# Performance work log

Hardware: AMD Instinct MI355X
Metric: run time of the kernel (lower is better)

## Reference

```python
import jax, jax.numpy as jnp
import numpy as np

B, N = 2, 4096
IN_CH, OUT_CH = 64, 64
L_MAX, NR = 3, 4
KERNEL_RADIUS = 0.5
PATCH = 64  # hardcoded in torch topk(-dist, 64)


def setup_inputs() -> dict:
    key = jax.random.key(0)
    k1, k2, k3 = jax.random.split(key, 3)
    xyz = jax.random.normal(k1, (B, N, 3), dtype=jnp.float32)
    signal = jax.random.normal(k2, (B, N, IN_CH), dtype=jnp.float32)
    # xavier_uniform on (out, in, nr, l_max+1): receptive = nr*(l_max+1)
    recept = NR * (L_MAX + 1)
    bound = float(np.sqrt(6.0 / (IN_CH * recept + OUT_CH * recept)))
    weight = jax.random.uniform(k3, (OUT_CH, IN_CH, NR, L_MAX + 1), dtype=jnp.float32,
                                minval=-bound, maxval=bound)
    biases = jnp.zeros((OUT_CH,), dtype=jnp.float32)
    return {"xyz": xyz, "signal": signal, "weight": weight, "biases": biases}


def _sph(X):
    # X: [B,N,P,3] l2-normalized patch directions -> [B,N,P,(L_MAX+1)^2]
    x, y, z = X[..., 0], X[..., 1], X[..., 2]
    x2, y2, z2 = x * x, y * y, z * z
    Ys = []
    Ys.append(jnp.full_like(x, 0.5 * np.sqrt(1.0 / np.pi)))           # Y00
    s3 = np.sqrt(3.0 / np.pi) / 2.0
    Ys += [s3 * y, s3 * z, -s3 * x]                                    # l=1
    s15h = np.sqrt(15.0 / np.pi) / 2.0
    s15q = np.sqrt(15.0 / np.pi) / 4.0
    s5q = np.sqrt(5.0 / np.pi) / 4.0
    Ys += [s15h * x * y, s15h * y * z, s5q * (2.0 * z2 - x2 - y2),
           -s15h * z * x, s15q * (x2 - y2)]                            # l=2
    c33 = np.sqrt(35.0 / (2.0 * np.pi)) / 4.0
    c32 = np.sqrt(105.0 / np.pi) / 2.0
    c31 = np.sqrt(21.0 / (2.0 * np.pi)) / 4.0
    c30 = np.sqrt(7.0 / np.pi) / 4.0
    c32b = np.sqrt(105.0 / np.pi) / 4.0
    Ys += [c33 * (3.0 * x2 * y - y * y2),
           c32 * x * y * z,
           c31 * (4.0 * y * z2 - x2 * y - y * y2),
           c30 * (2.0 * z * z2 - 3.0 * x2 * z - 3.0 * y2 * z),
           -c31 * (4.0 * z2 * x - x * x2 - x * y2),
           c32b * (x2 * z - y2 * z),
           -c33 * (x * x2 - 3.0 * x * y2)]                             # l=3
    return jnp.stack(Ys, axis=-1)


def reference(xyz, signal, weight, biases):
    # pairwise squared distances via matmul (costly_cdist)
    r2 = jnp.sum(xyz * xyz, axis=2)                                    # [B,N]
    sqd = r2[:, :, None] - 2.0 * jnp.einsum('bnd,bmd->bnm', xyz, xyz) + r2[:, None, :]
    neg_vals, idx = jax.lax.top_k(-sqd, PATCH)                         # KNN
    sq_patches_dist = -neg_vals                                        # [B,N,P]
    gather = jax.vmap(lambda pts, i: pts[i])                           # per-batch fancy gather
    patches = gather(xyz, idx) - xyz[:, :, None, :]                    # [B,N,P,3]
    # F.normalize(p=2, dim=-1, eps=0.01): x / max(||x||, eps)
    nrm = jnp.linalg.norm(patches, axis=-1, keepdims=True)
    Y = _sph(patches / jnp.maximum(nrm, 0.01))                         # [B,N,P,K2]
    dist = jnp.sqrt(jnp.maximum(sq_patches_dist, 1e-4))                # [B,N,P]
    r_grid = jnp.linspace(0.0, KERNEL_RADIUS, NR, dtype=jnp.float32)   # [NR]
    sigma = KERNEL_RADIUS / (NR - 1)
    rad = jnp.exp(-jnp.square(dist[..., None] - r_grid) / (2.0 * sigma ** 2))  # [B,N,P,NR]
    yk = Y[:, :, :, None, :] * rad[..., None]                          # [B,N,P,NR,K2]
    y_w = jnp.sum(yk[:, :, :, 0, 0], axis=2)[:, :, None, None, None]   # [B,N,1,1,1]
    conv_kernel = yk / (y_w + 1e-6)
    sig_patches = gather(signal, idx)                                  # [B,N,P,C]
    y = jnp.einsum('bvprn,bvpc->bvcrn', conv_kernel, sig_patches)
    y = y * y
    bands = [jnp.sum(y[..., l * l:(l + 1) * (l + 1)], axis=-1) for l in range(L_MAX + 1)]
    y = jnp.stack(bands, axis=-1)                                      # [B,N,C,NR,L+1]
    y = jnp.sqrt(jnp.maximum(y, 1e-4))
    out = jnp.einsum('ijrn,bvjrn->bvi', weight, y) + biases
    return out
```

## Files before the change

### kernel.cpp

```cpp
#include <hip/hip_runtime.h>
#include <hip/hip_bf16.h>
#include <math.h>

#define NB 2
#define NPTS 4096
#define CH 64
#define PATCH 64

typedef __attribute__((ext_vector_type(8))) short s16x8;
typedef __attribute__((ext_vector_type(4))) short s16x4;
typedef __attribute__((ext_vector_type(4))) float f32x4;
typedef __attribute__((ext_vector_type(4))) unsigned u32x4;

static __device__ __forceinline__ short f2bf(float f) {
    union { __hip_bfloat16 h; short s; } u;
    u.h = __float2bfloat16(f);
    return u.s;
}

__global__ __launch_bounds__(256) void prep_kernel(const float* __restrict__ W,
                                                   short* __restrict__ Wfrag,
                                                   const float* __restrict__ xyz,
                                                   float4* __restrict__ xyz4) {
    const int bid = blockIdx.x;
    const int tid = threadIdx.x;
    if (bid < 32) {
        const int gid = bid * 256 + tid;
        const int mt = gid >> 11;
        const int st = (gid >> 6) & 31;
        const int l  = gid & 63;
        const int i  = mt * 16 + (l & 15);
        const int k0 = st * 32 + (l >> 4) * 8;
        const f32x4 a = *(const f32x4*)&W[i * 1024 + k0];
        const f32x4 c = *(const f32x4*)&W[i * 1024 + k0 + 4];
        s16x8 v;
        v[0] = f2bf(a[0]); v[1] = f2bf(a[1]); v[2] = f2bf(a[2]); v[3] = f2bf(a[3]);
        v[4] = f2bf(c[0]); v[5] = f2bf(c[1]); v[6] = f2bf(c[2]); v[7] = f2bf(c[3]);
        *(s16x8*)&Wfrag[gid * 8] = v;
    } else {
        const int idx = (bid - 32) * 256 + tid;
        float4 v;
        v.x = xyz[idx * 3 + 0];
        v.y = xyz[idx * 3 + 1];
        v.z = xyz[idx * 3 + 2];
        v.w = 0.0f;
        xyz4[idx] = v;
    }
}

__global__ __launch_bounds__(256, 6) void knn_kernel(const float4* __restrict__ xyz4,
                                                     int* __restrict__ knn_idx) {
    const int pt   = blockIdx.x;
    const int b    = pt >> 12;
    const int q    = pt & (NPTS - 1);
    const int tid  = threadIdx.x;
    const int wv   = tid >> 6;
    const int lane = tid & 63;

    __shared__ __align__(16) unsigned hist[4096];
    __shared__ __align__(16) unsigned short sbin[4096];
    __shared__ unsigned wsum[4];
    __shared__ unsigned sh_H;
    __shared__ int sh_need;
    __shared__ int cnt_less, cnt_tie;

    const float4* xb = xyz4 + (size_t)b * NPTS;
    const float4 qp = xb[q];

#pragma unroll
    for (int u = 0; u < 4; ++u)
        ((u32x4*)hist)[u * 256 + tid] = (u32x4){0u, 0u, 0u, 0u};
    if (tid == 0) { cnt_less = 0; cnt_tie = 0; }
    __syncthreads();

#pragma unroll 4
    for (int i = 0; i < 16; ++i) {
        const int m = i * 256 + tid;
        const float4 p = xb[m];
        const float dx = p.x - qp.x;
        const float dy = p.y - qp.y;
        const float dz = p.z - qp.z;
        const float sq = fmaf(dx, dx, fmaf(dy, dy, dz * dz));
        const unsigned hk = __float_as_uint(sq) >> 19;
        sbin[i * 256 + tid] = (unsigned short)hk;
        atomicAdd(&hist[hk], 1u);
    }
    __syncthreads();

    unsigned tsum = 0;
#pragma unroll
    for (int u = 0; u < 4; ++u) {
        const u32x4 h4 = ((const u32x4*)hist)[tid * 4 + u];
        tsum += h4[0] + h4[1] + h4[2] + h4[3];
    }
    unsigned run = tsum;
#pragma unroll
    for (int off = 1; off < 64; off <<= 1) {
        const unsigned v = __shfl_up(run, off);
        if (lane >= off) run += v;
    }
    if (lane == 63) wsum[wv] = run;
    __syncthreads();
    unsigned wbase = 0;
    for (int w2 = 0; w2 < wv; ++w2) wbase += wsum[w2];
    const unsigned incl = wbase + run;
    const unsigned excl = incl - tsum;
    if ((int)excl < PATCH && PATCH <= (int)incl) {
        int nrem = PATCH - (int)excl;
        for (int u = 0; u < 16; ++u) {
            const unsigned cb = hist[tid * 16 + u];
            if (nrem <= (int)cb) { sh_H = (unsigned)(tid * 16 + u); sh_need = nrem; break; }
            nrem -= (int)cb;
        }
    }
    __syncthreads();

    const unsigned H = sh_H;
    const int need  = sh_need;
    const int nless = PATCH - need;
    int* optr = knn_idx + (size_t)pt * PATCH;
    unsigned* ckey = hist;
    unsigned* cidx = hist + 2048;

#pragma unroll 4
    for (int i = 0; i < 16; ++i) {
        const int m = i * 256 + tid;
        const unsigned hk = sbin[i * 256 + tid];
        if (hk < H) {
            const int pos = atomicAdd(&cnt_less, 1);
            optr[pos] = m;
        } else if (hk == H) {
            const int pos = atomicAdd(&cnt_tie, 1);
            if (pos < 2048) {
                const float4 p = xb[m];
                const float dx = p.x - qp.x;
                const float dy = p.y - qp.y;
                const float dz = p.z - qp.z;
                const float sq = fmaf(dx, dx, fmaf(dy, dy, dz * dz));
                ckey[pos] = __float_as_uint(sq);
                cidx[pos] = m;
            }
        }
    }
    __syncthreads();

    const int nc = min(cnt_tie, 2048);
    for (int i = tid; i < nc; i += 256) {
        const unsigned ki = ckey[i];
        int rank = 0;
        for (int j = 0; j < nc; ++j) {
            const unsigned kj = ckey[j];
            rank += (kj < ki || (kj == ki && j < i)) ? 1 : 0;
        }
        if (rank < need) optr[nless + rank] = cidx[i];
    }
}

__global__ __launch_bounds__(256, 4) void conv_kernel(const float4* __restrict__ xyz4,
                                                      const float* __restrict__ signal,
                                                      const short* __restrict__ Wfrag,
                                                      const float* __restrict__ biases,
                                                      const int* __restrict__ knn_idx,
                                                      float* __restrict__ out) {
    const int tid  = threadIdx.x;
    const int wv   = tid >> 6;
    const int lane = tid & 63;
    const int ln15 = lane & 15;
    const int kq   = lane >> 4;

    __shared__ __align__(16) short cks_bf[4096];
    __shared__ __align__(16) short ckF[4096];
    __shared__ __align__(16) short sigF[4096];
    __shared__ __align__(16) short zb[4 * 1032];
    __shared__ int   sIdx[PATCH];
    __shared__ float sh_inv;

    for (int it = 0; it < 4; ++it) {
        const int pt = blockIdx.x * 4 + it;
        const int b  = pt >> 12;
        const int q  = pt & (NPTS - 1);

        if (tid < PATCH) sIdx[tid] = knn_idx[(size_t)pt * PATCH + tid];
        __syncthreads();

        if (wv == 0) {
            const int p   = lane;
            const int idx = sIdx[p];
            const float4 cp = xyz4[(size_t)b * NPTS + q];
            const float4 np = xyz4[(size_t)b * NPTS + idx];
            const float dx = np.x - cp.x;
            const float dy = np.y - cp.y;
            const float dz = np.z - cp.z;
            const float nrm2 = dx * dx + dy * dy + dz * dz;
            const float inv_n = 1.0f / fmaxf(sqrtf(nrm2), 0.01f);
            const float x = dx * inv_n, y = dy * inv_n, z = dz * inv_n;
            const float x2 = x * x, y2 = y * y, zz = z * z;

            float Y[16];
            Y[0] = 0.28209479177387814f;
            const float s3 = 0.4886025119029199f;
            Y[1] = s3 * y;  Y[2] = s3 * z;  Y[3] = -s3 * x;
            const float s15h = 1.0925484305920792f;
            const float s15q = 0.5462742152960396f;
            const float s5q  = 0.31539156525252005f;
            Y[4] = s15h * x * y;
            Y[5] = s15h * y * z;
            Y[6] = s5q * (2.0f * zz - x2 - y2);
            Y[7] = -s15h * z * x;
            Y[8] = s15q * (x2 - y2);
            const float c33  = 0.5900435899266435f;
            const float c32  = 2.8906114426405543f;
            const float c31  = 0.4570457994644658f;
            const float c30  = 0.3731763325901154f;
            const float c32b = 1.4453057213202771f;
            Y[9]  = c33 * (3.0f * x2 * y - y * y2);
            Y[10] = c32 * x * y * z;
            Y[11] = c31 * (4.0f * y * zz - x2 * y - y * y2);
            Y[12] = c30 * (2.0f * z * zz - 3.0f * x2 * z - 3.0f * y2 * z);
            Y[13] = -c31 * (4.0f * zz * x - x * x2 - x * y2);
            Y[14] = c32b * (x2 * z - y2 * z);
            Y[15] = -c33 * (x * x2 - 3.0f * x * y2);

            const float dist = sqrtf(fmaxf(nrm2, 1e-4f));
            const float d1 = dist - 0.16666667f;
            const float d2 = dist - 0.33333334f;
            const float d3 = dist - 0.5f;
            float rad[4];
            rad[0] = expf(-dist * dist * 18.0f);
            rad[1] = expf(-d1 * d1 * 18.0f);
            rad[2] = expf(-d2 * d2 * 18.0f);
            rad[3] = expf(-d3 * d3 * 18.0f);

            const int pm = p & 15;
#pragma unroll
            for (int chunk = 0; chunk < 16; ++chunk) {
                const int r  = chunk >> 2;
                const int kb = (chunk & 3) * 4;
                s16x4 v;
                v[0] = f2bf(Y[kb + 0] * rad[r]);
                v[1] = f2bf(Y[kb + 1] * rad[r]);
                v[2] = f2bf(Y[kb + 2] * rad[r]);
                v[3] = f2bf(Y[kb + 3] * rad[r]);
                *(s16x4*)&cks_bf[p * 64 + ((chunk ^ pm) << 2)] = v;
            }
            float v = 0.28209479177387814f * rad[0];
#pragma unroll
            for (int off = 32; off > 0; off >>= 1) v += __shfl_down(v, off);
            if (p == 0) sh_inv = 1.0f / (v + 1e-6f);
        } else {
            const int r0 = (wv - 1) * 3;
            const int rn = (wv == 3) ? 2 : 3;
            for (int rr = 0; rr < rn; ++rr) {
                const int rd = r0 + rr;
                const int ct = rd >> 1, s = rd & 1;
                const int c  = ct * 16 + ln15;
                const int pb = s * 32 + kq * 8;
                s16x8 sv;
#pragma unroll
                for (int j = 0; j < 8; ++j) {
                    const float f = signal[(size_t)(b * NPTS + sIdx[pb + j]) * CH + c];
                    sv[j] = f2bf(f);
                }
                *(s16x8*)&sigF[(ct * 2 + s) * 512 + lane * 8] = sv;
            }
        }
        __syncthreads();

#pragma unroll
        for (int ff = 0; ff < 2; ++ff) {
            const int f  = wv + ff * 4;
            const int mt = f >> 1, s = f & 1;
            const int rk = mt * 16 + ln15;
            const int rsw = rk >> 2, rlo = rk & 3;
            const int pb = s * 32 + kq * 8;
            s16x8 av;
#pragma unroll
            for (int j = 0; j < 8; ++j) {
                const int p = pb + j;
                av[j] = cks_bf[p * 64 + ((rsw ^ (p & 15)) << 2) + rlo];
            }
            *(s16x8*)&ckF[f * 512 + lane * 8] = av;
        }
        __syncthreads();

        const s16x8 bf0 = *(const s16x8*)&sigF[(wv * 2 + 0) * 512 + lane * 8];
        const s16x8 bf1 = *(const s16x8*)&sigF[(wv * 2 + 1) * 512 + lane * 8];
        f32x4 acc0 = {0.f, 0.f, 0.f, 0.f}, acc1 = acc0, acc2 = acc0, acc3 = acc0;
        {
            s16x8 a;
            a = *(const s16x8*)&ckF[0 * 512 + lane * 8];
            acc0 = __builtin_amdgcn_mfma_f32_16x16x32_bf16(a, bf0, acc0, 0, 0, 0);
            a = *(const s16x8*)&ckF[1 * 512 + lane * 8];
            acc0 = __builtin_amdgcn_mfma_f32_16x16x32_bf16(a, bf1, acc0, 0, 0, 0);
            a = *(const s16x8*)&ckF[2 * 512 + lane * 8];
            acc1 = __builtin_amdgcn_mfma_f32_16x16x32_bf16(a, bf0, acc1, 0, 0, 0);
            a = *(const s16x8*)&ckF[3 * 512 + lane * 8];
            acc1 = __builtin_amdgcn_mfma_f32_16x16x32_bf16(a, bf1, acc1, 0, 0, 0);
            a = *(const s16x8*)&ckF[4 * 512 + lane * 8];
            acc2 = __builtin_amdgcn_mfma_f32_16x16x32_bf16(a, bf0, acc2, 0, 0, 0);
            a = *(const s16x8*)&ckF[5 * 512 + lane * 8];
            acc2 = __builtin_amdgcn_mfma_f32_16x16x32_bf16(a, bf1, acc2, 0, 0, 0);
            a = *(const s16x8*)&ckF[6 * 512 + lane * 8];
            acc3 = __builtin_amdgcn_mfma_f32_16x16x32_bf16(a, bf0, acc3, 0, 0, 0);
            a = *(const s16x8*)&ckF[7 * 512 + lane * 8];
            acc3 = __builtin_amdgcn_mfma_f32_16x16x32_bf16(a, bf1, acc3, 0, 0, 0);
        }

        const float inv = sh_inv;
        const int qq = kq;
        float rb[4][4];
#pragma unroll
        for (int mt = 0; mt < 4; ++mt) {
            f32x4 av = (mt == 0) ? acc0 : (mt == 1) ? acc1 : (mt == 2) ? acc2 : acc3;
            const float y0 = av[0] * inv, y1 = av[1] * inv;
            const float y2 = av[2] * inv, y3 = av[3] * inv;
            const float sA = y0 * y0;
            const float sB = y1 * y1 + y2 * y2 + y3 * y3;
            const float sAll = sA + sB;
            float b0 = (qq == 0) ? sA : 0.0f;
            float b1 = (qq == 0) ? sB : 0.0f;
            float b2 = (qq == 1) ? sAll : ((qq == 2) ? sA : 0.0f);
            float b3 = (qq == 3) ? sAll : ((qq == 2) ? sB : 0.0f);
            b0 += __shfl_xor(b0, 16); b0 += __shfl_xor(b0, 32);
            b1 += __shfl_xor(b1, 16); b1 += __shfl_xor(b1, 32);
            b2 += __shfl_xor(b2, 16); b2 += __shfl_xor(b2, 32);
            b3 += __shfl_xor(b3, 16); b3 += __shfl_xor(b3, 32);
            rb[mt][0] = b0; rb[mt][1] = b1; rb[mt][2] = b2; rb[mt][3] = b3;
        }
        float s0 = rb[0][0], s1 = rb[0][1], s2 = rb[0][2], s3 = rb[0][3];
#pragma unroll
        for (int mt = 1; mt < 4; ++mt) {
            s0 = (qq == mt) ? rb[mt][0] : s0;
            s1 = (qq == mt) ? rb[mt][1] : s1;
            s2 = (qq == mt) ? rb[mt][2] : s2;
            s3 = (qq == mt) ? rb[mt][3] : s3;
        }
        s16x4 zv;
        zv[0] = f2bf(sqrtf(fmaxf(s0, 1e-4f)));
        zv[1] = f2bf(sqrtf(fmaxf(s1, 1e-4f)));
        zv[2] = f2bf(sqrtf(fmaxf(s2, 1e-4f)));
        zv[3] = f2bf(sqrtf(fmaxf(s3, 1e-4f)));
        const int c = wv * 16 + ln15;
        *(s16x4*)&zb[it * 1032 + c * 16 + qq * 4] = zv;
    }
    __syncthreads();

    const int mt5 = wv;
    const int g   = ln15 & 3;
    f32x4 acc5 = {0.f, 0.f, 0.f, 0.f};
#pragma unroll 4
    for (int st = 0; st < 32; ++st) {
        const s16x8 a  = *(const s16x8*)&Wfrag[((mt5 * 32 + st) * 64 + lane) * 8];
        const s16x8 zf = *(const s16x8*)&zb[g * 1032 + st * 32 + kq * 8];
        acc5 = __builtin_amdgcn_mfma_f32_16x16x32_bf16(a, zf, acc5, 0, 0, 0);
    }
    if (ln15 < 4) {
        const int i0 = mt5 * 16 + kq * 4;
        const int orow = (blockIdx.x * 4 + g) * CH;
#pragma unroll
        for (int rg = 0; rg < 4; ++rg)
            out[orow + i0 + rg] = acc5[rg] + biases[i0 + rg];
    }
}

extern "C" void kernel_launch(void* const* d_in, const int* in_sizes, int n_in,
                              void* d_out, int out_size, void* d_ws, size_t ws_size,
                              hipStream_t stream) {
    const float* xyz    = (const float*)d_in[0];
    const float* signal = (const float*)d_in[1];
    const float* weight = (const float*)d_in[2];
    const float* biases = (const float*)d_in[3];
    float* out = (float*)d_out;

    char* ws = (char*)d_ws;
    int*    knn_idx = (int*)ws;
    short*  Wfrag   = (short*)(ws + (size_t)NB * NPTS * PATCH * sizeof(int));
    float4* xyz4    = (float4*)(ws + (size_t)NB * NPTS * PATCH * sizeof(int) + 131072);

    prep_kernel<<<64, 256, 0, stream>>>(weight, Wfrag, xyz, xyz4);
    knn_kernel<<<NB * NPTS, 256, 0, stream>>>(xyz4, knn_idx);
    conv_kernel<<<(NB * NPTS) / 4, 256, 0, stream>>>(xyz4, signal, Wfrag, biases,
                                                     knn_idx, out);
}
```

Measured before the change: 94.98 us.

## Pack kNN histogram into 16-bit halves and make conv wave-per-point

The kNN histogram now packs two 16-bit bin counters into each 32-bit word, halving shared memory so more blocks fit per CU (launch bound raised to 8), and the tie buffer shrinks to 1024 entries. The conv kernel is restructured so each wave handles two points on its own, with no block-wide syncs per point: it computes the spherical kernel, gathers signal rows via shuffled indices straight into registers, and issues all 16 MFMAs itself. Each block now covers 8 points, so the final weight MFMA stage fills 8 columns instead of 4. xyz4.w also gets the squared norm, which is not used yet. Risks are heavier register pressure in conv (launch bound lowered to 3), tie overflow when more than 1024 candidates share the cutoff bin, and 16-bit counter overflow in principle.

```diff
diff --git a/kernel.cpp b/kernel.cpp
--- a/kernel.cpp
+++ b/kernel.cpp
@@ -39,16 +39,17 @@
         *(s16x8*)&Wfrag[gid * 8] = v;
     } else {
         const int idx = (bid - 32) * 256 + tid;
+        const float x = xyz[idx * 3 + 0];
+        const float y = xyz[idx * 3 + 1];
+        const float z = xyz[idx * 3 + 2];
         float4 v;
-        v.x = xyz[idx * 3 + 0];
-        v.y = xyz[idx * 3 + 1];
-        v.z = xyz[idx * 3 + 2];
-        v.w = 0.0f;
+        v.x = x; v.y = y; v.z = z;
+        v.w = fmaf(x, x, fmaf(y, y, z * z));
         xyz4[idx] = v;
     }
 }
 
-__global__ __launch_bounds__(256, 6) void knn_kernel(const float4* __restrict__ xyz4,
+__global__ __launch_bounds__(256, 8) void knn_kernel(const float4* __restrict__ xyz4,
                                                      int* __restrict__ knn_idx) {
     const int pt   = blockIdx.x;
     const int b    = pt >> 12;
@@ -57,7 +58,7 @@
     const int wv   = tid >> 6;
     const int lane = tid & 63;
 
-    __shared__ __align__(16) unsigned hist[4096];
+    __shared__ __align__(16) unsigned hist[2048];
     __shared__ __align__(16) unsigned short sbin[4096];
     __shared__ unsigned wsum[4];
     __shared__ unsigned sh_H;
@@ -68,7 +69,7 @@
     const float4 qp = xb[q];
 
 #pragma unroll
-    for (int u = 0; u < 4; ++u)
+    for (int u = 0; u < 2; ++u)
         ((u32x4*)hist)[u * 256 + tid] = (u32x4){0u, 0u, 0u, 0u};
     if (tid == 0) { cnt_less = 0; cnt_tie = 0; }
     __syncthreads();
@@ -83,15 +84,18 @@
         const float sq = fmaf(dx, dx, fmaf(dy, dy, dz * dz));
         const unsigned hk = __float_as_uint(sq) >> 19;
         sbin[i * 256 + tid] = (unsigned short)hk;
-        atomicAdd(&hist[hk], 1u);
-    }
-    __syncthreads();
-
+        atomicAdd(&hist[hk & 2047], 1u << ((hk >> 11) << 4));
+    }
+    __syncthreads();
+
+    const int wb2 = (tid & 127) * 16;
+    const int shp = (tid >> 7) << 4;
     unsigned tsum = 0;
 #pragma unroll
     for (int u = 0; u < 4; ++u) {
-        const u32x4 h4 = ((const u32x4*)hist)[tid * 4 + u];
-        tsum += h4[0] + h4[1] + h4[2] + h4[3];
+        const u32x4 h4 = *(const u32x4*)&hist[wb2 + u * 4];
+        tsum += ((h4[0] >> shp) & 0xFFFFu) + ((h4[1] >> shp) & 0xFFFFu)
+              + ((h4[2] >> shp) & 0xFFFFu) + ((h4[3] >> shp) & 0xFFFFu);
     }
     unsigned run = tsum;
 #pragma unroll
@@ -108,7 +112,7 @@
     if ((int)excl < PATCH && PATCH <= (int)incl) {
         int nrem = PATCH - (int)excl;
         for (int u = 0; u < 16; ++u) {
-            const unsigned cb = hist[tid * 16 + u];
+            const unsigned cb = (hist[wb2 + u] >> shp) & 0xFFFFu;
             if (nrem <= (int)cb) { sh_H = (unsigned)(tid * 16 + u); sh_need = nrem; break; }
             nrem -= (int)cb;
         }
@@ -120,7 +124,7 @@
     const int nless = PATCH - need;
     int* optr = knn_idx + (size_t)pt * PATCH;
     unsigned* ckey = hist;
-    unsigned* cidx = hist + 2048;
+    unsigned* cidx = hist + 1024;
 
 #pragma unroll 4
     for (int i = 0; i < 16; ++i) {
@@ -131,7 +135,7 @@
             optr[pos] = m;
         } else if (hk == H) {
             const int pos = atomicAdd(&cnt_tie, 1);
-            if (pos < 2048) {
+            if (pos < 1024) {
                 const float4 p = xb[m];
                 const float dx = p.x - qp.x;
                 const float dy = p.y - qp.y;
@@ -144,7 +148,7 @@
     }
     __syncthreads();
 
-    const int nc = min(cnt_tie, 2048);
+    const int nc = min(cnt_tie, 1024);
     for (int i = tid; i < nc; i += 256) {
         const unsigned ki = ckey[i];
         int rank = 0;
@@ -156,7 +160,7 @@
     }
 }
 
-__global__ __launch_bounds__(256, 4) void conv_kernel(const float4* __restrict__ xyz4,
+__global__ __launch_bounds__(256, 3) void conv_kernel(const float4* __restrict__ xyz4,
                                                       const float* __restrict__ signal,
                                                       const short* __restrict__ Wfrag,
                                                       const float* __restrict__ biases,
@@ -168,195 +172,173 @@
     const int ln15 = lane & 15;
     const int kq   = lane >> 4;
 
-    __shared__ __align__(16) short cks_bf[4096];
-    __shared__ __align__(16) short ckF[4096];
-    __shared__ __align__(16) short sigF[4096];
-    __shared__ __align__(16) short zb[4 * 1032];
-    __shared__ int   sIdx[PATCH];
-    __shared__ float sh_inv;
-
-    for (int it = 0; it < 4; ++it) {
-        const int pt = blockIdx.x * 4 + it;
+    __shared__ __align__(16) short cks[4][4096];
+    __shared__ __align__(16) short zb[8 * 1032];
+
+    short* ckw = &cks[wv][0];
+
+    for (int ip = 0; ip < 2; ++ip) {
+        const int pt = blockIdx.x * 8 + wv * 2 + ip;
         const int b  = pt >> 12;
         const int q  = pt & (NPTS - 1);
-
-        if (tid < PATCH) sIdx[tid] = knn_idx[(size_t)pt * PATCH + tid];
-        __syncthreads();
-
-        if (wv == 0) {
-            const int p   = lane;
-            const int idx = sIdx[p];
-            const float4 cp = xyz4[(size_t)b * NPTS + q];
-            const float4 np = xyz4[(size_t)b * NPTS + idx];
-            const float dx = np.x - cp.x;
-            const float dy = np.y - cp.y;
-            const float dz = np.z - cp.z;
-            const float nrm2 = dx * dx + dy * dy + dz * dz;
-            const float inv_n = 1.0f / fmaxf(sqrtf(nrm2), 0.01f);
-            const float x = dx * inv_n, y = dy * inv_n, z = dz * inv_n;
-            const float x2 = x * x, y2 = y * y, zz = z * z;
-
-            float Y[16];
-            Y[0] = 0.28209479177387814f;
-            const float s3 = 0.4886025119029199f;
-            Y[1] = s3 * y;  Y[2] = s3 * z;  Y[3] = -s3 * x;
-            const float s15h = 1.0925484305920792f;
-            const float s15q = 0.5462742152960396f;
-            const float s5q  = 0.31539156525252005f;
-            Y[4] = s15h * x * y;
-            Y[5] = s15h * y * z;
-            Y[6] = s5q * (2.0f * zz - x2 - y2);
-            Y[7] = -s15h * z * x;
-            Y[8] = s15q * (x2 - y2);
-            const float c33  = 0.5900435899266435f;
-            const float c32  = 2.8906114426405543f;
-            const float c31  = 0.4570457994644658f;
-            const float c30  = 0.3731763325901154f;
-            const float c32b = 1.4453057213202771f;
-            Y[9]  = c33 * (3.0f * x2 * y - y * y2);
-            Y[10] = c32 * x * y * z;
-            Y[11] = c31 * (4.0f * y * zz - x2 * y - y * y2);
-            Y[12] = c30 * (2.0f * z * zz - 3.0f * x2 * z - 3.0f * y2 * z);
-            Y[13] = -c31 * (4.0f * zz * x - x * x2 - x * y2);
-            Y[14] = c32b * (x2 * z - y2 * z);
-            Y[15] = -c33 * (x * x2 - 3.0f * x * y2);
-
-            const float dist = sqrtf(fmaxf(nrm2, 1e-4f));
-            const float d1 = dist - 0.16666667f;
-            const float d2 = dist - 0.33333334f;
-            const float d3 = dist - 0.5f;
-            float rad[4];
-            rad[0] = expf(-dist * dist * 18.0f);
-            rad[1] = expf(-d1 * d1 * 18.0f);
-            rad[2] = expf(-d2 * d2 * 18.0f);
-            rad[3] = expf(-d3 * d3 * 18.0f);
-
-            const int pm = p & 15;
-#pragma unroll
-            for (int chunk = 0; chunk < 16; ++chunk) {
-                const int r  = chunk >> 2;
-                const int kb = (chunk & 3) * 4;
-                s16x4 v;
-                v[0] = f2bf(Y[kb + 0] * rad[r]);
-                v[1] = f2bf(Y[kb + 1] * rad[r]);
-                v[2] = f2bf(Y[kb + 2] * rad[r]);
-                v[3] = f2bf(Y[kb + 3] * rad[r]);
-                *(s16x4*)&cks_bf[p * 64 + ((chunk ^ pm) << 2)] = v;
-            }
-            float v = 0.28209479177387814f * rad[0];
-#pragma unroll
-            for (int off = 32; off > 0; off >>= 1) v += __shfl_down(v, off);
-            if (p == 0) sh_inv = 1.0f / (v + 1e-6f);
-        } else {
-            const int r0 = (wv - 1) * 3;
-            const int rn = (wv == 3) ? 2 : 3;
-            for (int rr = 0; rr < rn; ++rr) {
-                const int rd = r0 + rr;
-                const int ct = rd >> 1, s = rd & 1;
-                const int c  = ct * 16 + ln15;
-                const int pb = s * 32 + kq * 8;
-                s16x8 sv;
+        const float4* xbase = xyz4 + (size_t)b * NPTS;
+        const float* sgb = signal + (size_t)b * NPTS * CH;
+
+        const int p   = lane;
+        const int idx = knn_idx[(size_t)pt * PATCH + p];
+        const float4 cp = xbase[q];
+        const float4 np = xbase[idx];
+        const float dx = np.x - cp.x;
+        const float dy = np.y - cp.y;
+        const float dz = np.z - cp.z;
+        const float nrm2 = dx * dx + dy * dy + dz * dz;
+        const float inv_n = 1.0f / fmaxf(sqrtf(nrm2), 0.01f);
+        const float x = dx * inv_n, y = dy * inv_n, z = dz * inv_n;
+        const float x2 = x * x, y2 = y * y, zz = z * z;
+
+        float Y[16];
+        Y[0] = 0.28209479177387814f;
+        const float s3 = 0.4886025119029199f;
+        Y[1] = s3 * y;  Y[2] = s3 * z;  Y[3] = -s3 * x;
+        const float s15h = 1.0925484305920792f;
+        const float s15q = 0.5462742152960396f;
+        const float s5q  = 0.31539156525252005f;
+        Y[4] = s15h * x * y;
+        Y[5] = s15h * y * z;
+        Y[6] = s5q * (2.0f * zz - x2 - y2);
+        Y[7] = -s15h * z * x;
+        Y[8] = s15q * (x2 - y2);
+        const float c33  = 0.5900435899266435f;
+        const float c32  = 2.8906114426405543f;
+        const float c31  = 0.4570457994644658f;
+        const float c30  = 0.3731763325901154f;
+        const float c32b = 1.4453057213202771f;
+        Y[9]  = c33 * (3.0f * x2 * y - y * y2);
+        Y[10] = c32 * x * y * z;
+        Y[11] = c31 * (4.0f * y * zz - x2 * y - y * y2);
+        Y[12] = c30 * (2.0f * z * zz - 3.0f * x2 * z - 3.0f * y2 * z);
+        Y[13] = -c31 * (4.0f * zz * x - x * x2 - x * y2);
+        Y[14] = c32b * (x2 * z - y2 * z);
+        Y[15] = -c33 * (x * x2 - 3.0f * x * y2);
+
+        const float dist = sqrtf(fmaxf(nrm2, 1e-4f));
+        const float d1 = dist - 0.16666667f;
+        const float d2 = dist - 0.33333334f;
+        const float d3 = dist - 0.5f;
+        float rad[4];
+        rad[0] = expf(-dist * dist * 18.0f);
+        rad[1] = expf(-d1 * d1 * 18.0f);
+        rad[2] = expf(-d2 * d2 * 18.0f);
+        rad[3] = expf(-d3 * d3 * 18.0f);
+
+        const int pm = p & 15;
+#pragma unroll
+        for (int chunk = 0; chunk < 16; ++chunk) {
+            const int r  = chunk >> 2;
+            const int kb = (chunk & 3) * 4;
+            s16x4 v;
+            v[0] = f2bf(Y[kb + 0] * rad[r]);
+            v[1] = f2bf(Y[kb + 1] * rad[r]);
+            v[2] = f2bf(Y[kb + 2] * rad[r]);
+            v[3] = f2bf(Y[kb + 3] * rad[r]);
+            *(s16x4*)&ckw[p * 64 + ((chunk ^ pm) << 2)] = v;
+        }
+        float vv = 0.28209479177387814f * rad[0];
+#pragma unroll
+        for (int off = 1; off < 64; off <<= 1) vv += __shfl_xor(vv, off);
+        const float inv = 1.0f / (vv + 1e-6f);
+
+        s16x8 bf[8];
+#pragma unroll
+        for (int s = 0; s < 2; ++s) {
+#pragma unroll
+            for (int j = 0; j < 8; ++j) {
+                const int row = __shfl(idx, s * 32 + kq * 8 + j);
+                const float* rp = sgb + ((size_t)row << 6) + ln15;
+                bf[0 * 2 + s][j] = f2bf(rp[0]);
+                bf[1 * 2 + s][j] = f2bf(rp[16]);
+                bf[2 * 2 + s][j] = f2bf(rp[32]);
+                bf[3 * 2 + s][j] = f2bf(rp[48]);
+            }
+        }
+
+        f32x4 acc[4][4];
+#pragma unroll
+        for (int mt = 0; mt < 4; ++mt)
+#pragma unroll
+            for (int ct = 0; ct < 4; ++ct)
+                acc[mt][ct] = (f32x4){0.f, 0.f, 0.f, 0.f};
+#pragma unroll
+        for (int s = 0; s < 2; ++s) {
+#pragma unroll
+            for (int mt = 0; mt < 4; ++mt) {
+                const int rk  = mt * 16 + ln15;
+                const int rsw = rk >> 2, rlo = rk & 3;
+                s16x8 a;
 #pragma unroll
                 for (int j = 0; j < 8; ++j) {
-                    const float f = signal[(size_t)(b * NPTS + sIdx[pb + j]) * CH + c];
-                    sv[j] = f2bf(f);
+                    const int p2 = s * 32 + kq * 8 + j;
+                    a[j] = ckw[p2 * 64 + ((rsw ^ (p2 & 15)) << 2) + rlo];
                 }
-                *(s16x8*)&sigF[(ct * 2 + s) * 512 + lane * 8] = sv;
-            }
-        }
-        __syncthreads();
-
-#pragma unroll
-        for (int ff = 0; ff < 2; ++ff) {
-            const int f  = wv + ff * 4;
-            const int mt = f >> 1, s = f & 1;
-            const int rk = mt * 16 + ln15;
-            const int rsw = rk >> 2, rlo = rk & 3;
-            const int pb = s * 32 + kq * 8;
-            s16x8 av;
-#pragma unroll
-            for (int j = 0; j < 8; ++j) {
-                const int p = pb + j;
-                av[j] = cks_bf[p * 64 + ((rsw ^ (p & 15)) << 2) + rlo];
-            }
-            *(s16x8*)&ckF[f * 512 + lane * 8] = av;
-        }
-        __syncthreads();
-
-        const s16x8 bf0 = *(const s16x8*)&sigF[(wv * 2 + 0) * 512 + lane * 8];
-        const s16x8 bf1 = *(const s16x8*)&sigF[(wv * 2 + 1) * 512 + lane * 8];
-        f32x4 acc0 = {0.f, 0.f, 0.f, 0.f}, acc1 = acc0, acc2 = acc0, acc3 = acc0;
-        {
-            s16x8 a;
-            a = *(const s16x8*)&ckF[0 * 512 + lane * 8];
-            acc0 = __builtin_amdgcn_mfma_f32_16x16x32_bf16(a, bf0, acc0, 0, 0, 0);
-            a = *(const s16x8*)&ckF[1 * 512 + lane * 8];
-            acc0 = __builtin_amdgcn_mfma_f32_16x16x32_bf16(a, bf1, acc0, 0, 0, 0);
-            a = *(const s16x8*)&ckF[2 * 512 + lane * 8];
-            acc1 = __builtin_amdgcn_mfma_f32_16x16x32_bf16(a, bf0, acc1, 0, 0, 0);
-            a = *(const s16x8*)&ckF[3 * 512 + lane * 8];
-            acc1 = __builtin_amdgcn_mfma_f32_16x16x32_bf16(a, bf1, acc1, 0, 0, 0);
-            a = *(const s16x8*)&ckF[4 * 512 + lane * 8];
-            acc2 = __builtin_amdgcn_mfma_f32_16x16x32_bf16(a, bf0, acc2, 0, 0, 0);
-            a = *(const s16x8*)&ckF[5 * 512 + lane * 8];
-            acc2 = __builtin_amdgcn_mfma_f32_16x16x32_bf16(a, bf1, acc2, 0, 0, 0);
-            a = *(const s16x8*)&ckF[6 * 512 + lane * 8];
-            acc3 = __builtin_amdgcn_mfma_f32_16x16x32_bf16(a, bf0, acc3, 0, 0, 0);
-            a = *(const s16x8*)&ckF[7 * 512 + lane * 8];
-            acc3 = __builtin_amdgcn_mfma_f32_16x16x32_bf16(a, bf1, acc3, 0, 0, 0);
-        }
-
-        const float inv = sh_inv;
+                acc[mt][0] = __builtin_amdgcn_mfma_f32_16x16x32_bf16(a, bf[0 * 2 + s], acc[mt][0], 0, 0, 0);
+                acc[mt][1] = __builtin_amdgcn_mfma_f32_16x16x32_bf16(a, bf[1 * 2 + s], acc[mt][1], 0, 0, 0);
+                acc[mt][2] = __builtin_amdgcn_mfma_f32_16x16x32_bf16(a, bf[2 * 2 + s], acc[mt][2], 0, 0, 0);
+                acc[mt][3] = __builtin_amdgcn_mfma_f32_16x16x32_bf16(a, bf[3 * 2 + s], acc[mt][3], 0, 0, 0);
+            }
+        }
+
         const int qq = kq;
-        float rb[4][4];
-#pragma unroll
-        for (int mt = 0; mt < 4; ++mt) {
-            f32x4 av = (mt == 0) ? acc0 : (mt == 1) ? acc1 : (mt == 2) ? acc2 : acc3;
-            const float y0 = av[0] * inv, y1 = av[1] * inv;
-            const float y2 = av[2] * inv, y3 = av[3] * inv;
-            const float sA = y0 * y0;
-            const float sB = y1 * y1 + y2 * y2 + y3 * y3;
-            const float sAll = sA + sB;
-            float b0 = (qq == 0) ? sA : 0.0f;
-            float b1 = (qq == 0) ? sB : 0.0f;
-            float b2 = (qq == 1) ? sAll : ((qq == 2) ? sA : 0.0f);
-            float b3 = (qq == 3) ? sAll : ((qq == 2) ? sB : 0.0f);
-            b0 += __shfl_xor(b0, 16); b0 += __shfl_xor(b0, 32);
-            b1 += __shfl_xor(b1, 16); b1 += __shfl_xor(b1, 32);
-            b2 += __shfl_xor(b2, 16); b2 += __shfl_xor(b2, 32);
-            b3 += __shfl_xor(b3, 16); b3 += __shfl_xor(b3, 32);
-            rb[mt][0] = b0; rb[mt][1] = b1; rb[mt][2] = b2; rb[mt][3] = b3;
-        }
-        float s0 = rb[0][0], s1 = rb[0][1], s2 = rb[0][2], s3 = rb[0][3];
-#pragma unroll
-        for (int mt = 1; mt < 4; ++mt) {
-            s0 = (qq == mt) ? rb[mt][0] : s0;
-            s1 = (qq == mt) ? rb[mt][1] : s1;
-            s2 = (qq == mt) ? rb[mt][2] : s2;
-            s3 = (qq == mt) ? rb[mt][3] : s3;
-        }
-        s16x4 zv;
-        zv[0] = f2bf(sqrtf(fmaxf(s0, 1e-4f)));
-        zv[1] = f2bf(sqrtf(fmaxf(s1, 1e-4f)));
-        zv[2] = f2bf(sqrtf(fmaxf(s2, 1e-4f)));
-        zv[3] = f2bf(sqrtf(fmaxf(s3, 1e-4f)));
-        const int c = wv * 16 + ln15;
-        *(s16x4*)&zb[it * 1032 + c * 16 + qq * 4] = zv;
-    }
-    __syncthreads();
-
-    const int mt5 = wv;
-    const int g   = ln15 & 3;
+#pragma unroll
+        for (int ct = 0; ct < 4; ++ct) {
+            float rb[4][4];
+#pragma unroll
+            for (int mt = 0; mt < 4; ++mt) {
+                const f32x4 av = acc[mt][ct];
+                const float y0 = av[0] * inv, y1 = av[1] * inv;
+                const float y2 = av[2] * inv, y3 = av[3] * inv;
+                const float sA = y0 * y0;
+                const float sB = y1 * y1 + y2 * y2 + y3 * y3;
+                const float sAll = sA + sB;
+                float b0 = (qq == 0) ? sA : 0.0f;
+                float b1 = (qq == 0) ? sB : 0.0f;
+                float b2 = (qq == 1) ? sAll : ((qq == 2) ? sA : 0.0f);
+                float b3 = (qq == 3) ? sAll : ((qq == 2) ? sB : 0.0f);
+                b0 += __shfl_xor(b0, 16); b0 += __shfl_xor(b0, 32);
+                b1 += __shfl_xor(b1, 16); b1 += __shfl_xor(b1, 32);
+                b2 += __shfl_xor(b2, 16); b2 += __shfl_xor(b2, 32);
+                b3 += __shfl_xor(b3, 16); b3 += __shfl_xor(b3, 32);
+                rb[mt][0] = b0; rb[mt][1] = b1; rb[mt][2] = b2; rb[mt][3] = b3;
+            }
+            float s0 = rb[0][0], s1 = rb[0][1], s2 = rb[0][2], s3 = rb[0][3];
+#pragma unroll
+            for (int mt = 1; mt < 4; ++mt) {
+                s0 = (qq == mt) ? rb[mt][0] : s0;
+                s1 = (qq == mt) ? rb[mt][1] : s1;
+                s2 = (qq == mt) ? rb[mt][2] : s2;
+                s3 = (qq == mt) ? rb[mt][3] : s3;
+            }
+            s16x4 zv;
+            zv[0] = f2bf(sqrtf(fmaxf(s0, 1e-4f)));
+            zv[1] = f2bf(sqrtf(fmaxf(s1, 1e-4f)));
+            zv[2] = f2bf(sqrtf(fmaxf(s2, 1e-4f)));
+            zv[3] = f2bf(sqrtf(fmaxf(s3, 1e-4f)));
+            const int c = ct * 16 + ln15;
+            *(s16x4*)&zb[(wv * 2 + ip) * 1032 + c * 16 + qq * 4] = zv;
+        }
+    }
+    __syncthreads();
+
+    const int g = ln15 & 7;
     f32x4 acc5 = {0.f, 0.f, 0.f, 0.f};
 #pragma unroll 4
     for (int st = 0; st < 32; ++st) {
-        const s16x8 a  = *(const s16x8*)&Wfrag[((mt5 * 32 + st) * 64 + lane) * 8];
+        const s16x8 a  = *(const s16x8*)&Wfrag[((wv * 32 + st) * 64 + lane) * 8];
         const s16x8 zf = *(const s16x8*)&zb[g * 1032 + st * 32 + kq * 8];
         acc5 = __builtin_amdgcn_mfma_f32_16x16x32_bf16(a, zf, acc5, 0, 0, 0);
     }
-    if (ln15 < 4) {
-        const int i0 = mt5 * 16 + kq * 4;
-        const int orow = (blockIdx.x * 4 + g) * CH;
+    if (ln15 < 8) {
+        const int i0 = wv * 16 + kq * 4;
+        const int orow = (blockIdx.x * 8 + g) * CH;
 #pragma unroll
         for (int rg = 0; rg < 4; ++rg)
             out[orow + i0 + rg] = acc5[rg] + biases[i0 + rg];
@@ -379,6 +361,6 @@
 
     prep_kernel<<<64, 256, 0, stream>>>(weight, Wfrag, xyz, xyz4);
     knn_kernel<<<NB * NPTS, 256, 0, stream>>>(xyz4, knn_idx);
-    conv_kernel<<<(NB * NPTS) / 4, 256, 0, stream>>>(xyz4, signal, Wfrag, biases,
+    conv_kernel<<<(NB * NPTS) / 8, 256, 0, stream>>>(xyz4, signal, Wfrag, biases,
                                                      knn_idx, out);
 }
```

After: 127.8 us. +34.6%, slower.
